# Optimization experiments

Measured on AMD Instinct MI355X. Metric: run time of the kernel, lower is better.

## Reference

```python
import jax, jax.numpy as jnp
import numpy as np
import math

D = 768
H = 8
DK = D // H
FF = 1024
EPS = 1e-5


def _layer_norm(x, g, b):
    m = jnp.mean(x, axis=-1, keepdims=True)
    v = jnp.mean((x - m) ** 2, axis=-1, keepdims=True)
    return (x - m) * jax.lax.rsqrt(v + EPS) * g + b


def _mha(x, attention_mask, Wq, bq, Wv, bv, g, b):
    # x: (B,S,D); attention_mask: (B,S,1) bool (True = masked/padding query row)
    B, S, _ = x.shape
    q = (x @ Wq + bq).reshape(B, S, H, DK).transpose(0, 2, 1, 3)  # (B,H,S,dk)
    # NOTE: original code uses the V projection for BOTH k and v (k = self.V(x))
    kv = (x @ Wv + bv).reshape(B, S, H, DK).transpose(0, 2, 1, 3)
    k = kv
    v = kv
    w = jnp.einsum('bhqd,bhkd->bhqk', q, k) / math.sqrt(DK)  # (B,H,S,S)
    pad = attention_mask[:, None, :, :]                      # (B,1,S,1) -> bcast (B,1,S,S)
    causal = jnp.triu(jnp.ones((S, S), dtype=bool), k=1)     # look-ahead mask
    mask = pad | causal
    w = jnp.where(mask, jnp.float32(-1e9), w)
    # NOTE: original uses nn.Softmax(dim=2) -> softmax over the QUERY axis
    score = jax.nn.softmax(w, axis=2)
    o = jnp.einsum('bhqk,bhkd->bhqd', score, v)              # (B,H,S,dk)
    o = o.transpose(0, 2, 1, 3).reshape(B, S, D)
    return _layer_norm(o + x, g, b)


def _ffn(x, W1, b1, W2, b2, g, b):
    h = jax.nn.relu(x @ W1 + b1)
    return _layer_norm(h @ W2 + b2 + x, g, b)


def setup_inputs() -> dict:
    key = jax.random.key(0)
    ks = jax.random.split(key, 16)
    B, S = 8, 1024
    sc = 0.02
    inp = {
        'x': jax.random.normal(ks[0], (B, S, D), dtype=jnp.float32),
        'attention_mask': jax.random.randint(ks[1], (B, S, 1), 0, 2).astype(bool),
    }
    for i, pre in enumerate(['a1', 'a2']):
        inp[pre + '_Wq'] = jax.random.normal(ks[2 + 4 * i], (D, D), dtype=jnp.float32) * sc
        inp[pre + '_bq'] = jnp.zeros((D,), dtype=jnp.float32)
        inp[pre + '_Wv'] = jax.random.normal(ks[3 + 4 * i], (D, D), dtype=jnp.float32) * sc
        inp[pre + '_bv'] = jnp.zeros((D,), dtype=jnp.float32)
        inp[pre + '_g'] = jnp.ones((D,), dtype=jnp.float32)
        inp[pre + '_b'] = jnp.zeros((D,), dtype=jnp.float32)
    inp['f_W1'] = jax.random.normal(ks[10], (D, FF), dtype=jnp.float32) * sc
    inp['f_b1'] = jnp.zeros((FF,), dtype=jnp.float32)
    inp['f_W2'] = jax.random.normal(ks[11], (FF, D), dtype=jnp.float32) * sc
    inp['f_b2'] = jnp.zeros((D,), dtype=jnp.float32)
    inp['f_g'] = jnp.ones((D,), dtype=jnp.float32)
    inp['f_b'] = jnp.zeros((D,), dtype=jnp.float32)
    return inp


def reference(x, attention_mask,
              a1_Wq, a1_bq, a1_Wv, a1_bv, a1_g, a1_b,
              a2_Wq, a2_bq, a2_Wv, a2_bv, a2_g, a2_b,
              f_W1, f_b1, f_W2, f_b2, f_g, f_b):
    x = _mha(x, attention_mask, a1_Wq, a1_bq, a1_Wv, a1_bv, a1_g, a1_b)
    x = _mha(x, attention_mask, a2_Wq, a2_bq, a2_Wv, a2_bv, a2_g, a2_b)
    x = _ffn(x, f_W1, f_b1, f_W2, f_b2, f_g, f_b)
    return x
```

## Files before the change

### kernel.cpp

```cpp
#include <hip/hip_runtime.h>
#include <cstddef>

#define BB 8
#define SS 1024
#define DD 768
#define HH 8
#define DKK 96
#define FFF 1024
#define MM (BB*SS)
#define QVW 1536
#define SM_SCALE 0.10206207261596577f
#define NTILES 16
#define NPAIR  136

typedef unsigned short ushort_t;
typedef short short8 __attribute__((ext_vector_type(8)));
typedef float f32x4 __attribute__((ext_vector_type(4)));
typedef ushort_t us4 __attribute__((ext_vector_type(4)));

__device__ __forceinline__ ushort_t f2b(float f) {
    union { float f; unsigned u; } x; x.f = f;
    unsigned r = x.u + 0x7fffu + ((x.u >> 16) & 1u);
    return (ushort_t)(r >> 16);
}
__device__ __forceinline__ float b2f(ushort_t u) {
    union { unsigned u; float f; } x; x.u = ((unsigned)u) << 16;
    return x.f;
}
__device__ __forceinline__ void gload16(const ushort_t* g, void* lds_base) {
    __builtin_amdgcn_global_load_lds(
        (const __attribute__((address_space(1))) unsigned int*)g,
        (__attribute__((address_space(3))) unsigned int*)lds_base, 16, 0, 0);
}

__global__ __launch_bounds__(256) void castWT(
    const float* __restrict__ W, ushort_t* __restrict__ Wt, int K, int N)
{
    __shared__ float T[32][33];
    const int tx = threadIdx.x & 31, ty = threadIdx.x >> 5;
    const int n0 = blockIdx.x * 32, k0 = blockIdx.y * 32;
    #pragma unroll
    for (int r = 0; r < 4; ++r)
        T[ty + 8*r][tx] = W[(size_t)(k0 + ty + 8*r) * N + n0 + tx];
    __syncthreads();
    #pragma unroll
    for (int r = 0; r < 4; ++r)
        Wt[(size_t)(n0 + ty + 8*r) * K + k0 + tx] = f2b(T[tx][ty + 8*r]);
}

__global__ __launch_bounds__(256) void castWT4(
    const float* __restrict__ Wa, const float* __restrict__ Wb,
    const float* __restrict__ Wc, const float* __restrict__ Wd,
    ushort_t* __restrict__ Ta, ushort_t* __restrict__ Tb,
    ushort_t* __restrict__ Tc, ushort_t* __restrict__ Td)
{
    __shared__ float T[32][33];
    const float* W; ushort_t* Wt;
    switch (blockIdx.z) {
        case 0:  W = Wa; Wt = Ta; break;
        case 1:  W = Wb; Wt = Tb; break;
        case 2:  W = Wc; Wt = Tc; break;
        default: W = Wd; Wt = Td; break;
    }
    const int tx = threadIdx.x & 31, ty = threadIdx.x >> 5;
    const int n0 = blockIdx.x * 32, k0 = blockIdx.y * 32;
    #pragma unroll
    for (int r = 0; r < 4; ++r)
        T[ty + 8*r][tx] = W[(size_t)(k0 + ty + 8*r) * DD + n0 + tx];
    __syncthreads();
    #pragma unroll
    for (int r = 0; r < 4; ++r)
        Wt[(size_t)(n0 + ty + 8*r) * DD + k0 + tx] = f2b(T[tx][ty + 8*r]);
}

__global__ __launch_bounds__(256) void cast_f2b(
    const float* __restrict__ in, ushort_t* __restrict__ out, int n4)
{
    const int i = blockIdx.x * 256 + threadIdx.x;
    if (i >= n4) return;
    const float4 v = ((const float4*)in)[i];
    us4 o; o.x = f2b(v.x); o.y = f2b(v.y); o.z = f2b(v.z); o.w = f2b(v.w);
    ((us4*)out)[i] = o;
}

template<int RELU>
__global__ __launch_bounds__(256) void gemm_bt(
    const ushort_t* __restrict__ A, const ushort_t* __restrict__ Bt,
    const float* __restrict__ bias, const float* __restrict__ bias2, int bN,
    ushort_t* __restrict__ C, int K, int N)
{
    __shared__ ushort_t S[128*136];
    ushort_t* As = S;
    ushort_t* Bs = S + 128*64;
    const int tid  = threadIdx.x;
    const int lane = tid & 63, wave = tid >> 6;
    const int wm = wave >> 1, wn = wave & 1;
    const int n = lane & 15, quad = lane >> 4;
    const int sx = n & 7;
    const int bm = blockIdx.y * 128, bn = blockIdx.x * 128;

    f32x4 acc[4][4];
    #pragma unroll
    for (int i = 0; i < 4; ++i)
        #pragma unroll
        for (int j = 0; j < 4; ++j) acc[i][j] = (f32x4){0.f, 0.f, 0.f, 0.f};

    for (int k0 = 0; k0 < K; k0 += 64) {
        #pragma unroll
        for (int it = 0; it < 4; ++it) {
            const int u   = (it*4 + wave)*64 + lane;
            const int row = u >> 3;
            const int c   = (u & 7) ^ (row & 7);
            gload16(A  + (size_t)(bm + row) * K + k0 + c*8, (char*)As + (it*4 + wave)*1024);
            gload16(Bt + (size_t)(bn + row) * K + k0 + c*8, (char*)Bs + (it*4 + wave)*1024);
        }
        __syncthreads();
        #pragma unroll
        for (int ks = 0; ks < 2; ++ks) {
            short8 af[4], bf[4];
            #pragma unroll
            for (int i = 0; i < 4; ++i)
                af[i] = *(short8*)&As[((wm*64 + i*16 + n)*8 + ((ks*4 + quad) ^ sx))*8];
            #pragma unroll
            for (int j = 0; j < 4; ++j)
                bf[j] = *(short8*)&Bs[((wn*64 + j*16 + n)*8 + ((ks*4 + quad) ^ sx))*8];
            #pragma unroll
            for (int i = 0; i < 4; ++i)
                #pragma unroll
                for (int j = 0; j < 4; ++j)
                    acc[i][j] = __builtin_amdgcn_mfma_f32_16x16x32_bf16(af[i], bf[j], acc[i][j], 0, 0, 0);
        }
        __syncthreads();
    }
    #pragma unroll
    for (int j = 0; j < 4; ++j) {
        const int col = wn*64 + j*16 + n;
        const int gcol = bn + col;
        const float bsv = (gcol < bN) ? bias[gcol] : bias2[gcol - bN];
        #pragma unroll
        for (int i = 0; i < 4; ++i) {
            const int lrow = wm*64 + i*16 + quad*4;
            #pragma unroll
            for (int r = 0; r < 4; ++r) {
                float v = acc[i][j][r] + bsv;
                if (RELU) v = fmaxf(v, 0.f);
                S[(lrow + r)*136 + col] = f2b(v);
            }
        }
    }
    __syncthreads();
    #pragma unroll
    for (int it = 0; it < 8; ++it) {
        const int u = it*256 + tid;
        const int grow = u >> 4, gc = u & 15;
        *(short8*)(C + (size_t)(bm + grow)*N + bn + gc*8) = *(short8*)&S[grow*136 + gc*8];
    }
}

__global__ __launch_bounds__(256) void attn_sums(
    const ushort_t* __restrict__ QV, const int* __restrict__ amask,
    float* __restrict__ lpart)
{
    __shared__ ushort_t Qs[64*128];
    __shared__ ushort_t Ks[64*128];
    __shared__ float colsum[4][64];
    __shared__ float padf[64];
    const int tid = threadIdx.x, lane = tid & 63, wave = tid >> 6;
    const int n = lane & 15, quad = lane >> 4;
    const int sx = n & 7;
    const int t = blockIdx.x;
    int qt = (int)((-1.f + sqrtf(1.f + 8.f*(float)t)) * 0.5f);
    if ((qt+1)*(qt+2)/2 <= t) ++qt;
    if (qt*(qt+1)/2 > t) --qt;
    const int kt = t - qt*(qt+1)/2;
    const int q0 = qt*64, k0 = kt*64;
    const int h = blockIdx.y, b = blockIdx.z;
    const ushort_t* Qh = QV + (size_t)b*SS*QVW + h*DKK;
    const ushort_t* Kh = QV + (size_t)b*SS*QVW + DD + h*DKK;

    #pragma unroll
    for (int it = 0; it < 4; ++it) {
        const int u = (it*4 + wave)*64 + lane;
        const int row = u >> 4;
        const int c = (u & 15) ^ (row & 7);
        if (c < 12) {
            gload16(Qh + (size_t)(q0 + row)*QVW + c*8, (char*)Qs + (it*4 + wave)*1024);
            gload16(Kh + (size_t)(k0 + row)*QVW + c*8, (char*)Ks + (it*4 + wave)*1024);
        }
    }
    if (tid < 64) padf[tid] = (amask[b*SS + q0 + tid] != 0) ? 1.f : 0.f;
    __syncthreads();

    #pragma unroll
    for (int ns = 0; ns < 4; ++ns) {
        f32x4 sa = (f32x4){0.f, 0.f, 0.f, 0.f};
        #pragma unroll
        for (int ks = 0; ks < 3; ++ks) {
            const short8 aq = *(short8*)&Qs[((wave*16 + n)*16 + ((ks*4 + quad) ^ sx))*8];
            const short8 bk = *(short8*)&Ks[((ns*16   + n)*16 + ((ks*4 + quad) ^ sx))*8];
            sa = __builtin_amdgcn_mfma_f32_16x16x32_bf16(aq, bk, sa, 0, 0, 0);
        }
        const int kl = ns*16 + n;
        const int keyg = k0 + kl;
        float s = 0.f;
        #pragma unroll
        for (int r = 0; r < 4; ++r) {
            const int qrow = wave*16 + quad*4 + r;
            const bool dead = (padf[qrow] != 0.f) || (keyg > q0 + qrow);
            const float e = dead ? 0.f : __expf(sa[r] * SM_SCALE);
            s += e;
        }
        s += __shfl_xor(s, 16);
        s += __shfl_xor(s, 32);
        if (quad == 0) colsum[wave][kl] = s;
    }
    __syncthreads();
    if (tid < 64) {
        const float s = colsum[0][tid] + colsum[1][tid] + colsum[2][tid] + colsum[3][tid];
        lpart[((size_t)(b*HH + h)*NTILES + qt)*SS + k0 + tid] = s;
    }
}

__global__ __launch_bounds__(256) void transpose_scale(
    const ushort_t* __restrict__ QV, const float* __restrict__ lpart,
    ushort_t* __restrict__ Vt)
{
    __shared__ ushort_t T[64][104];
    __shared__ float rlv[64];
    const int tid = threadIdx.x;
    const int k0 = blockIdx.x * 64, h = blockIdx.y, b = blockIdx.z;
    const ushort_t* src = QV + (size_t)b*SS*QVW + DD + h*DKK;
    for (int s = tid; s < 768; s += 256) {
        const int r = s / 12, c = s % 12;
        *(short8*)&T[r][c*8] = *(const short8*)(src + (size_t)(k0 + r)*QVW + c*8);
    }
    if (tid < 64) {
        const float* lp = lpart + (size_t)(b*HH + h)*NTILES*SS;
        float l = 0.f;
        for (int qt = k0 >> 6; qt < NTILES; ++qt) l += lp[(size_t)qt*SS + k0 + tid];
        rlv[tid] = (l > 0.f) ? (1.f / l) : 0.f;
    }
    __syncthreads();
    ushort_t* dst = Vt + ((size_t)b*HH + h)*DKK*SS;
    for (int s = tid; s < 768; s += 256) {
        const int dk = s >> 3, c = s & 7;
        short8 v;
        #pragma unroll
        for (int i = 0; i < 8; ++i)
            v[i] = (short)f2b(b2f(T[c*8 + i][dk]) * rlv[c*8 + i]);
        *(short8*)(dst + (size_t)dk*SS + k0 + c*8) = v;
    }
}

__global__ __launch_bounds__(256) void attn_pv_re(
    const ushort_t* __restrict__ QV, const int* __restrict__ amask,
    const ushort_t* __restrict__ Vt, ushort_t* __restrict__ O)
{
    __shared__ ushort_t Qs[64*128];
    __shared__ ushort_t Ks[64*128];
    __shared__ ushort_t Vs[96*64];
    __shared__ ushort_t Es[64*64];
    __shared__ float padf[64];
    const int tid = threadIdx.x, lane = tid & 63, wave = tid >> 6;
    const int n = lane & 15, quad = lane >> 4;
    const int sx = n & 7;
    const int px = blockIdx.x;
    const int h = blockIdx.y, b = blockIdx.z;
    const ushort_t* Qh = QV + (size_t)b*SS*QVW + h*DKK;
    const ushort_t* Kh = QV + (size_t)b*SS*QVW + DD + h*DKK;
    const ushort_t* Vth = Vt + ((size_t)b*HH + h)*DKK*SS;

    #pragma unroll
    for (int half = 0; half < 2; ++half) {
        const int qt = half ? (15 - px) : px;
        const int q0 = qt * 64;

        #pragma unroll
        for (int it = 0; it < 4; ++it) {
            const int u = (it*4 + wave)*64 + lane;
            const int row = u >> 4;
            const int c = (u & 15) ^ (row & 7);
            if (c < 12)
                gload16(Qh + (size_t)(q0 + row)*QVW + c*8, (char*)Qs + (it*4 + wave)*1024);
        }
        if (tid < 64) padf[tid] = (amask[b*SS + q0 + tid] != 0) ? 1.f : 0.f;

        f32x4 acc[6];
        #pragma unroll
        for (int t = 0; t < 6; ++t) acc[t] = (f32x4){0.f, 0.f, 0.f, 0.f};

        for (int kt = 0; kt <= qt; ++kt) {
            const int k0 = kt * 64;
            #pragma unroll
            for (int it = 0; it < 4; ++it) {
                const int u = (it*4 + wave)*64 + lane;
                const int row = u >> 4;
                const int c = (u & 15) ^ (row & 7);
                if (c < 12)
                    gload16(Kh + (size_t)(k0 + row)*QVW + c*8, (char*)Ks + (it*4 + wave)*1024);
            }
            #pragma unroll
            for (int it = 0; it < 3; ++it) {
                const int u = (it*4 + wave)*64 + lane;
                const int row = u >> 3, c = (u & 7) ^ (row & 7);
                gload16(Vth + (size_t)row*SS + k0 + c*8, (char*)Vs + (it*4 + wave)*1024);
            }
            __syncthreads();

            #pragma unroll
            for (int ns = 0; ns < 4; ++ns) {
                f32x4 sa = (f32x4){0.f, 0.f, 0.f, 0.f};
                #pragma unroll
                for (int ks = 0; ks < 3; ++ks) {
                    const short8 aq = *(short8*)&Qs[((wave*16 + n)*16 + ((ks*4 + quad) ^ sx))*8];
                    const short8 bk = *(short8*)&Ks[((ns*16   + n)*16 + ((ks*4 + quad) ^ sx))*8];
                    sa = __builtin_amdgcn_mfma_f32_16x16x32_bf16(aq, bk, sa, 0, 0, 0);
                }
                const int kl = ns*16 + n;
                const int keyg = k0 + kl;
                #pragma unroll
                for (int r = 0; r < 4; ++r) {
                    const int lq = quad*4 + r;
                    const int trow = wave*16 + lq;
                    const bool dead = (padf[trow] != 0.f) || (keyg > q0 + trow);
                    const float e = dead ? 0.f : __expf(sa[r] * SM_SCALE);
                    Es[trow*64 + (((kl >> 3) ^ (lq & 7)) * 8) + (kl & 7)] = f2b(e);
                }
            }
            asm volatile("s_waitcnt lgkmcnt(0)" ::: "memory");
            __builtin_amdgcn_sched_barrier(0);

            #pragma unroll
            for (int kk = 0; kk < 2; ++kk) {
                const short8 ae = *(short8*)&Es[((wave*16 + n)*8 + ((kk*4 + quad) ^ sx))*8];
                #pragma unroll
                for (int nt = 0; nt < 6; ++nt) {
                    const short8 bv = *(short8*)&Vs[((nt*16 + n)*8 + ((kk*4 + quad) ^ sx))*8];
                    acc[nt] = __builtin_amdgcn_mfma_f32_16x16x32_bf16(ae, bv, acc[nt], 0, 0, 0);
                }
            }
            __syncthreads();
        }
        #pragma unroll
        for (int nt = 0; nt < 6; ++nt) {
            #pragma unroll
            for (int r = 0; r < 4; ++r) {
                const int q = q0 + wave*16 + quad*4 + r;
                O[((size_t)b*SS + q)*DD + h*DKK + nt*16 + n] = f2b(acc[nt][r]);
            }
        }
    }
}

__device__ __forceinline__ float block_sum256(float s, float* tmp4)
{
    #pragma unroll
    for (int off = 32; off > 0; off >>= 1) s += __shfl_down(s, off);
    __syncthreads();
    if ((threadIdx.x & 63) == 0) tmp4[threadIdx.x >> 6] = s;
    __syncthreads();
    return tmp4[0] + tmp4[1] + tmp4[2] + tmp4[3];
}

template<int XBF, int RBF, int OUTF32>
__global__ __launch_bounds__(256) void resid_ln(
    const void* __restrict__ X, const void* __restrict__ R,
    const float* __restrict__ g, const float* __restrict__ beta,
    ushort_t* __restrict__ OutB, float* __restrict__ OutF)
{
    __shared__ float tmp4[4];
    const int row = blockIdx.x;
    const int tid = threadIdx.x;
    float v[3], s = 0.f;
    #pragma unroll
    for (int i = 0; i < 3; ++i) {
        const size_t idx = (size_t)row * DD + tid + 256*i;
        const float xv = XBF ? b2f(((const ushort_t*)X)[idx]) : ((const float*)X)[idx];
        const float rv = RBF ? b2f(((const ushort_t*)R)[idx]) : ((const float*)R)[idx];
        v[i] = xv + rv;
        s += v[i];
    }
    const float mu = block_sum256(s, tmp4) * (1.f / DD);
    float qv = 0.f;
    #pragma unroll
    for (int i = 0; i < 3; ++i) { const float d = v[i] - mu; qv += d * d; }
    const float inv = rsqrtf(block_sum256(qv, tmp4) * (1.f / DD) + 1e-5f);
    #pragma unroll
    for (int i = 0; i < 3; ++i) {
        const int c = tid + 256*i;
        const float o = (v[i] - mu) * inv * g[c] + beta[c];
        if (OUTF32) OutF[(size_t)row * DD + c] = o;
        else        OutB[(size_t)row * DD + c] = f2b(o);
    }
}

extern "C" void kernel_launch(void* const* d_in, const int* in_sizes, int n_in,
                              void* d_out, int out_size, void* d_ws, size_t ws_size,
                              hipStream_t stream)
{
    (void)in_sizes; (void)n_in; (void)out_size; (void)ws_size;
    const float* x0    = (const float*)d_in[0];
    const int*   amask = (const int*)d_in[1];
    const float* a1_Wq = (const float*)d_in[2];
    const float* a1_bq = (const float*)d_in[3];
    const float* a1_Wv = (const float*)d_in[4];
    const float* a1_bv = (const float*)d_in[5];
    const float* a1_g  = (const float*)d_in[6];
    const float* a1_b  = (const float*)d_in[7];
    const float* a2_Wq = (const float*)d_in[8];
    const float* a2_bq = (const float*)d_in[9];
    const float* a2_Wv = (const float*)d_in[10];
    const float* a2_bv = (const float*)d_in[11];
    const float* a2_g  = (const float*)d_in[12];
    const float* a2_b  = (const float*)d_in[13];
    const float* f_W1  = (const float*)d_in[14];
    const float* f_b1  = (const float*)d_in[15];
    const float* f_W2  = (const float*)d_in[16];
    const float* f_b2  = (const float*)d_in[17];
    const float* f_g   = (const float*)d_in[18];
    const float* f_b   = (const float*)d_in[19];

    char* ws = (char*)d_ws;
    size_t off = 0;
    auto alloc = [&](size_t bytes) { void* p = ws + off; off += (bytes + 255) & ~(size_t)255; return p; };
    ushort_t* WqvT1 = (ushort_t*)alloc((size_t)QVW*DD*2);
    ushort_t* WqvT2 = (ushort_t*)alloc((size_t)QVW*DD*2);
    ushort_t* W1T   = (ushort_t*)alloc((size_t)DD*FFF*2);
    ushort_t* W2T   = (ushort_t*)alloc((size_t)DD*FFF*2);
    ushort_t* xb0   = (ushort_t*)alloc((size_t)MM*DD*2);
    ushort_t* xb1   = (ushort_t*)alloc((size_t)MM*DD*2);
    ushort_t* xb2   = (ushort_t*)alloc((size_t)MM*DD*2);
    ushort_t* Ob    = (ushort_t*)alloc((size_t)MM*DD*2);
    ushort_t* QVb   = (ushort_t*)alloc((size_t)MM*QVW*2);
    ushort_t* hb    = QVb;
    ushort_t* Vtb   = (ushort_t*)alloc((size_t)MM*DD*2);
    float* lpart = (float*)alloc((size_t)BB*HH*NTILES*SS*4);
    float* out = (float*)d_out;

    const dim3 blk(256);
    const dim3 gsc(NPAIR, HH, BB);
    const dim3 gpv(NTILES/2, HH, BB);
    const dim3 gtr(SS/64, HH, BB);
    const dim3 gqv(QVW/128, MM/128);
    const dim3 gf1(FFF/128, MM/128);
    const dim3 gf2(DD/128, MM/128);

    castWT4<<<dim3(DD/32, DD/32, 4), blk, 0, stream>>>(
        a1_Wq, a1_Wv, a2_Wq, a2_Wv,
        WqvT1, WqvT1 + (size_t)DD*DD, WqvT2, WqvT2 + (size_t)DD*DD);
    castWT<<<dim3(FFF/32, DD/32), blk, 0, stream>>>(f_W1, W1T, DD, FFF);
    castWT<<<dim3(DD/32, FFF/32), blk, 0, stream>>>(f_W2, W2T, FFF, DD);
    cast_f2b<<<(MM*DD/4 + 255)/256, blk, 0, stream>>>(x0, xb0, MM*DD/4);

    gemm_bt<0><<<gqv, blk, 0, stream>>>(xb0, WqvT1, a1_bq, a1_bv, DD, QVb, DD, QVW);
    attn_sums<<<gsc, blk, 0, stream>>>(QVb, amask, lpart);
    transpose_scale<<<gtr, blk, 0, stream>>>(QVb, lpart, Vtb);
    attn_pv_re<<<gpv, blk, 0, stream>>>(QVb, amask, Vtb, Ob);
    resid_ln<1,0,0><<<dim3(MM), blk, 0, stream>>>(Ob, x0, a1_g, a1_b, xb1, nullptr);

    gemm_bt<0><<<gqv, blk, 0, stream>>>(xb1, WqvT2, a2_bq, a2_bv, DD, QVb, DD, QVW);
    attn_sums<<<gsc, blk, 0, stream>>>(QVb, amask, lpart);
    transpose_scale<<<gtr, blk, 0, stream>>>(QVb, lpart, Vtb);
    attn_pv_re<<<gpv, blk, 0, stream>>>(QVb, amask, Vtb, Ob);
    resid_ln<1,1,0><<<dim3(MM), blk, 0, stream>>>(Ob, xb1, a2_g, a2_b, xb2, nullptr);

    gemm_bt<1><<<gf1, blk, 0, stream>>>(xb2, W1T, f_b1, f_b1, FFF, hb, DD, FFF);
    gemm_bt<0><<<gf2, blk, 0, stream>>>(hb, W2T, f_b2, f_b2, DD, Ob, FFF, DD);
    resid_ln<1,1,1><<<dim3(MM), blk, 0, stream>>>(Ob, xb2, f_g, f_b, nullptr, out);
}
```

Before: 433.1 us.

## Use 128-row query tiles with double-buffered K/V loads in attention kernels

Both attention kernels now process 128-query tiles with 512-thread blocks. Each block loops over 64-key tiles, double-buffering the K and V shared-memory loads so the next tile is fetched while the current one is computed. attn_sums moves from one block per (q,k) tile pair to a looped, paired causal schedule that matches attn_pv_re, with blockIdx remapped to spread heads across XCDs. This halves the partial-sum tiles and reuses Q fragments held in registers, at the cost of more LDS per block and possibly lower occupancy and fewer blocks (256).

```diff
diff --git a/kernel.cpp b/kernel.cpp
--- a/kernel.cpp
+++ b/kernel.cpp
@@ -10,8 +10,7 @@
 #define MM (BB*SS)
 #define QVW 1536
 #define SM_SCALE 0.10206207261596577f
-#define NTILES 16
-#define NPAIR  136
+#define NT2 8
 
 typedef unsigned short ushort_t;
 typedef short short8 __attribute__((ext_vector_type(8)));
@@ -157,67 +156,101 @@
     }
 }
 
-__global__ __launch_bounds__(256) void attn_sums(
+__global__ __launch_bounds__(512) void attn_sums(
     const ushort_t* __restrict__ QV, const int* __restrict__ amask,
     float* __restrict__ lpart)
 {
-    __shared__ ushort_t Qs[64*128];
-    __shared__ ushort_t Ks[64*128];
-    __shared__ float colsum[4][64];
-    __shared__ float padf[64];
+    __shared__ ushort_t Qs[128*128];
+    __shared__ ushort_t Ks[2][64*128];
+    __shared__ float colsum[2][8][64];
     const int tid = threadIdx.x, lane = tid & 63, wave = tid >> 6;
-    const int n = lane & 15, quad = lane >> 4;
-    const int sx = n & 7;
-    const int t = blockIdx.x;
-    int qt = (int)((-1.f + sqrtf(1.f + 8.f*(float)t)) * 0.5f);
-    if ((qt+1)*(qt+2)/2 <= t) ++qt;
-    if (qt*(qt+1)/2 > t) --qt;
-    const int kt = t - qt*(qt+1)/2;
-    const int q0 = qt*64, k0 = kt*64;
-    const int h = blockIdx.y, b = blockIdx.z;
+    const int n = lane & 15, quad = lane >> 4, sx = n & 7;
+    const int hwid = blockIdx.x;
+    const int v = (hwid & 7) * 32 + (hwid >> 3);
+    const int px = v & 3, h = (v >> 2) & 7, b = v >> 5;
     const ushort_t* Qh = QV + (size_t)b*SS*QVW + h*DKK;
     const ushort_t* Kh = QV + (size_t)b*SS*QVW + DD + h*DKK;
-
-    #pragma unroll
-    for (int it = 0; it < 4; ++it) {
-        const int u = (it*4 + wave)*64 + lane;
-        const int row = u >> 4;
-        const int c = (u & 15) ^ (row & 7);
-        if (c < 12) {
-            gload16(Qh + (size_t)(q0 + row)*QVW + c*8, (char*)Qs + (it*4 + wave)*1024);
-            gload16(Kh + (size_t)(k0 + row)*QVW + c*8, (char*)Ks + (it*4 + wave)*1024);
-        }
-    }
-    if (tid < 64) padf[tid] = (amask[b*SS + q0 + tid] != 0) ? 1.f : 0.f;
-    __syncthreads();
-
-    #pragma unroll
-    for (int ns = 0; ns < 4; ++ns) {
-        f32x4 sa = (f32x4){0.f, 0.f, 0.f, 0.f};
-        #pragma unroll
-        for (int ks = 0; ks < 3; ++ks) {
-            const short8 aq = *(short8*)&Qs[((wave*16 + n)*16 + ((ks*4 + quad) ^ sx))*8];
-            const short8 bk = *(short8*)&Ks[((ns*16   + n)*16 + ((ks*4 + quad) ^ sx))*8];
-            sa = __builtin_amdgcn_mfma_f32_16x16x32_bf16(aq, bk, sa, 0, 0, 0);
-        }
-        const int kl = ns*16 + n;
-        const int keyg = k0 + kl;
-        float s = 0.f;
-        #pragma unroll
-        for (int r = 0; r < 4; ++r) {
-            const int qrow = wave*16 + quad*4 + r;
-            const bool dead = (padf[qrow] != 0.f) || (keyg > q0 + qrow);
-            const float e = dead ? 0.f : __expf(sa[r] * SM_SCALE);
-            s += e;
-        }
-        s += __shfl_xor(s, 16);
-        s += __shfl_xor(s, 32);
-        if (quad == 0) colsum[wave][kl] = s;
-    }
-    __syncthreads();
-    if (tid < 64) {
-        const float s = colsum[0][tid] + colsum[1][tid] + colsum[2][tid] + colsum[3][tid];
-        lpart[((size_t)(b*HH + h)*NTILES + qt)*SS + k0 + tid] = s;
+    float* lpq = lpart + (size_t)(b*HH + h)*NT2*SS;
+
+    #pragma unroll
+    for (int half = 0; half < 2; ++half) {
+        const int qt2 = half ? (7 - px) : px;
+        const int q0 = qt2 * 128;
+        const int ktmax = 2*qt2 + 1;
+        #pragma unroll
+        for (int it = 0; it < 4; ++it) {
+            const int u = (it*8 + wave)*64 + lane;
+            const int row = u >> 4, c = (u & 15) ^ (row & 7);
+            if (c < 12)
+                gload16(Qh + (size_t)(q0 + row)*QVW + c*8, (char*)Qs + (it*8 + wave)*1024);
+        }
+        const int4 mv = *(const int4*)&amask[b*SS + q0 + wave*16 + quad*4];
+        const int mr[4] = {mv.x, mv.y, mv.z, mv.w};
+        #pragma unroll
+        for (int it = 0; it < 2; ++it) {
+            const int u = (it*8 + wave)*64 + lane;
+            const int row = u >> 4, c = (u & 15) ^ (row & 7);
+            if (c < 12)
+                gload16(Kh + (size_t)row*QVW + c*8, (char*)Ks[0] + (it*8 + wave)*1024);
+        }
+        __syncthreads();
+        short8 aq[3];
+        #pragma unroll
+        for (int ks = 0; ks < 3; ++ks)
+            aq[ks] = *(short8*)&Qs[((wave*16 + n)*16 + ((ks*4 + quad) ^ sx))*8];
+
+        int cur = 0;
+        for (int kt = 0; kt <= ktmax; ++kt) {
+            const int k0 = kt * 64;
+            if (kt < ktmax) {
+                #pragma unroll
+                for (int it = 0; it < 2; ++it) {
+                    const int u = (it*8 + wave)*64 + lane;
+                    const int row = u >> 4, c = (u & 15) ^ (row & 7);
+                    if (c < 12)
+                        gload16(Kh + (size_t)(k0 + 64 + row)*QVW + c*8,
+                                (char*)Ks[cur^1] + (it*8 + wave)*1024);
+                }
+            }
+            if (kt > 0 && tid < 64) {
+                const float s = colsum[cur^1][0][tid] + colsum[cur^1][1][tid]
+                              + colsum[cur^1][2][tid] + colsum[cur^1][3][tid]
+                              + colsum[cur^1][4][tid] + colsum[cur^1][5][tid]
+                              + colsum[cur^1][6][tid] + colsum[cur^1][7][tid];
+                lpq[(size_t)qt2*SS + (k0 - 64) + tid] = s;
+            }
+            #pragma unroll
+            for (int ns = 0; ns < 4; ++ns) {
+                f32x4 sa = (f32x4){0.f, 0.f, 0.f, 0.f};
+                #pragma unroll
+                for (int ks = 0; ks < 3; ++ks) {
+                    const short8 bk = *(short8*)&Ks[cur][((ns*16 + n)*16 + ((ks*4 + quad) ^ sx))*8];
+                    sa = __builtin_amdgcn_mfma_f32_16x16x32_bf16(aq[ks], bk, sa, 0, 0, 0);
+                }
+                const int kl = ns*16 + n;
+                const int keyg = k0 + kl;
+                float s = 0.f;
+                #pragma unroll
+                for (int r = 0; r < 4; ++r) {
+                    const int qg = q0 + wave*16 + quad*4 + r;
+                    const bool dead = (mr[r] != 0) || (keyg > qg);
+                    s += dead ? 0.f : __expf(sa[r] * SM_SCALE);
+                }
+                s += __shfl_xor(s, 16);
+                s += __shfl_xor(s, 32);
+                if (quad == 0) colsum[cur][wave][kl] = s;
+            }
+            __syncthreads();
+            cur ^= 1;
+        }
+        if (tid < 64) {
+            const int pb = ktmax & 1;
+            const float s = colsum[pb][0][tid] + colsum[pb][1][tid]
+                          + colsum[pb][2][tid] + colsum[pb][3][tid]
+                          + colsum[pb][4][tid] + colsum[pb][5][tid]
+                          + colsum[pb][6][tid] + colsum[pb][7][tid];
+            lpq[(size_t)qt2*SS + ktmax*64 + tid] = s;
+        }
     }
 }
 
@@ -235,9 +268,9 @@
         *(short8*)&T[r][c*8] = *(const short8*)(src + (size_t)(k0 + r)*QVW + c*8);
     }
     if (tid < 64) {
-        const float* lp = lpart + (size_t)(b*HH + h)*NTILES*SS;
+        const float* lp = lpart + (size_t)(b*HH + h)*NT2*SS;
         float l = 0.f;
-        for (int qt = k0 >> 6; qt < NTILES; ++qt) l += lp[(size_t)qt*SS + k0 + tid];
+        for (int qt2 = k0 >> 7; qt2 < NT2; ++qt2) l += lp[(size_t)qt2*SS + k0 + tid];
         rlv[tid] = (l > 0.f) ? (1.f / l) : 0.f;
     }
     __syncthreads();
@@ -252,69 +285,91 @@
     }
 }
 
-__global__ __launch_bounds__(256) void attn_pv_re(
+__global__ __launch_bounds__(512) void attn_pv_re(
     const ushort_t* __restrict__ QV, const int* __restrict__ amask,
     const ushort_t* __restrict__ Vt, ushort_t* __restrict__ O)
 {
-    __shared__ ushort_t Qs[64*128];
-    __shared__ ushort_t Ks[64*128];
-    __shared__ ushort_t Vs[96*64];
-    __shared__ ushort_t Es[64*64];
-    __shared__ float padf[64];
+    __shared__ ushort_t Qs[128*128];
+    __shared__ ushort_t Ks[2][64*128];
+    __shared__ ushort_t Vs[2][96*64];
+    __shared__ ushort_t Es[128*64];
     const int tid = threadIdx.x, lane = tid & 63, wave = tid >> 6;
-    const int n = lane & 15, quad = lane >> 4;
-    const int sx = n & 7;
-    const int px = blockIdx.x;
-    const int h = blockIdx.y, b = blockIdx.z;
+    const int n = lane & 15, quad = lane >> 4, sx = n & 7;
+    const int hwid = blockIdx.x;
+    const int v = (hwid & 7) * 32 + (hwid >> 3);
+    const int px = v & 3, h = (v >> 2) & 7, b = v >> 5;
     const ushort_t* Qh = QV + (size_t)b*SS*QVW + h*DKK;
     const ushort_t* Kh = QV + (size_t)b*SS*QVW + DD + h*DKK;
     const ushort_t* Vth = Vt + ((size_t)b*HH + h)*DKK*SS;
 
     #pragma unroll
     for (int half = 0; half < 2; ++half) {
-        const int qt = half ? (15 - px) : px;
-        const int q0 = qt * 64;
-
+        const int qt2 = half ? (7 - px) : px;
+        const int q0 = qt2 * 128;
+        const int ktmax = 2*qt2 + 1;
         #pragma unroll
         for (int it = 0; it < 4; ++it) {
-            const int u = (it*4 + wave)*64 + lane;
-            const int row = u >> 4;
-            const int c = (u & 15) ^ (row & 7);
+            const int u = (it*8 + wave)*64 + lane;
+            const int row = u >> 4, c = (u & 15) ^ (row & 7);
             if (c < 12)
-                gload16(Qh + (size_t)(q0 + row)*QVW + c*8, (char*)Qs + (it*4 + wave)*1024);
-        }
-        if (tid < 64) padf[tid] = (amask[b*SS + q0 + tid] != 0) ? 1.f : 0.f;
+                gload16(Qh + (size_t)(q0 + row)*QVW + c*8, (char*)Qs + (it*8 + wave)*1024);
+        }
+        const int4 mv = *(const int4*)&amask[b*SS + q0 + wave*16 + quad*4];
+        const int mr[4] = {mv.x, mv.y, mv.z, mv.w};
+        #pragma unroll
+        for (int it = 0; it < 2; ++it) {
+            const int u = (it*8 + wave)*64 + lane;
+            const int row = u >> 4, c = (u & 15) ^ (row & 7);
+            if (c < 12)
+                gload16(Kh + (size_t)row*QVW + c*8, (char*)Ks[0] + (it*8 + wave)*1024);
+        }
+        #pragma unroll
+        for (int it = 0; it < 2; ++it) {
+            if (it*8 + wave < 12) {
+                const int u = (it*8 + wave)*64 + lane;
+                const int row = u >> 3, c = (u & 7) ^ (row & 7);
+                gload16(Vth + (size_t)row*SS + c*8, (char*)Vs[0] + (it*8 + wave)*1024);
+            }
+        }
+        __syncthreads();
+        short8 aq[3];
+        #pragma unroll
+        for (int ks = 0; ks < 3; ++ks)
+            aq[ks] = *(short8*)&Qs[((wave*16 + n)*16 + ((ks*4 + quad) ^ sx))*8];
 
         f32x4 acc[6];
         #pragma unroll
         for (int t = 0; t < 6; ++t) acc[t] = (f32x4){0.f, 0.f, 0.f, 0.f};
 
-        for (int kt = 0; kt <= qt; ++kt) {
+        int cur = 0;
+        for (int kt = 0; kt <= ktmax; ++kt) {
             const int k0 = kt * 64;
-            #pragma unroll
-            for (int it = 0; it < 4; ++it) {
-                const int u = (it*4 + wave)*64 + lane;
-                const int row = u >> 4;
-                const int c = (u & 15) ^ (row & 7);
-                if (c < 12)
-                    gload16(Kh + (size_t)(k0 + row)*QVW + c*8, (char*)Ks + (it*4 + wave)*1024);
-            }
-            #pragma unroll
-            for (int it = 0; it < 3; ++it) {
-                const int u = (it*4 + wave)*64 + lane;
-                const int row = u >> 3, c = (u & 7) ^ (row & 7);
-                gload16(Vth + (size_t)row*SS + k0 + c*8, (char*)Vs + (it*4 + wave)*1024);
-            }
-            __syncthreads();
-
+            if (kt < ktmax) {
+                #pragma unroll
+                for (int it = 0; it < 2; ++it) {
+                    const int u = (it*8 + wave)*64 + lane;
+                    const int row = u >> 4, c = (u & 15) ^ (row & 7);
+                    if (c < 12)
+                        gload16(Kh + (size_t)(k0 + 64 + row)*QVW + c*8,
+                                (char*)Ks[cur^1] + (it*8 + wave)*1024);
+                }
+                #pragma unroll
+                for (int it = 0; it < 2; ++it) {
+                    if (it*8 + wave < 12) {
+                        const int u = (it*8 + wave)*64 + lane;
+                        const int row = u >> 3, c = (u & 7) ^ (row & 7);
+                        gload16(Vth + (size_t)row*SS + k0 + 64 + c*8,
+                                (char*)Vs[cur^1] + (it*8 + wave)*1024);
+                    }
+                }
+            }
             #pragma unroll
             for (int ns = 0; ns < 4; ++ns) {
                 f32x4 sa = (f32x4){0.f, 0.f, 0.f, 0.f};
                 #pragma unroll
                 for (int ks = 0; ks < 3; ++ks) {
-                    const short8 aq = *(short8*)&Qs[((wave*16 + n)*16 + ((ks*4 + quad) ^ sx))*8];
-                    const short8 bk = *(short8*)&Ks[((ns*16   + n)*16 + ((ks*4 + quad) ^ sx))*8];
-                    sa = __builtin_amdgcn_mfma_f32_16x16x32_bf16(aq, bk, sa, 0, 0, 0);
+                    const short8 bk = *(short8*)&Ks[cur][((ns*16 + n)*16 + ((ks*4 + quad) ^ sx))*8];
+                    sa = __builtin_amdgcn_mfma_f32_16x16x32_bf16(aq[ks], bk, sa, 0, 0, 0);
                 }
                 const int kl = ns*16 + n;
                 const int keyg = k0 + kl;
@@ -322,7 +377,7 @@
                 for (int r = 0; r < 4; ++r) {
                     const int lq = quad*4 + r;
                     const int trow = wave*16 + lq;
-                    const bool dead = (padf[trow] != 0.f) || (keyg > q0 + trow);
+                    const bool dead = (mr[r] != 0) || (keyg > q0 + trow);
                     const float e = dead ? 0.f : __expf(sa[r] * SM_SCALE);
                     Es[trow*64 + (((kl >> 3) ^ (lq & 7)) * 8) + (kl & 7)] = f2b(e);
                 }
@@ -335,11 +390,12 @@
                 const short8 ae = *(short8*)&Es[((wave*16 + n)*8 + ((kk*4 + quad) ^ sx))*8];
                 #pragma unroll
                 for (int nt = 0; nt < 6; ++nt) {
-                    const short8 bv = *(short8*)&Vs[((nt*16 + n)*8 + ((kk*4 + quad) ^ sx))*8];
+                    const short8 bv = *(short8*)&Vs[cur][((nt*16 + n)*8 + ((kk*4 + quad) ^ sx))*8];
                     acc[nt] = __builtin_amdgcn_mfma_f32_16x16x32_bf16(ae, bv, acc[nt], 0, 0, 0);
                 }
             }
             __syncthreads();
+            cur ^= 1;
         }
         #pragma unroll
         for (int nt = 0; nt < 6; ++nt) {
@@ -434,12 +490,12 @@
     ushort_t* QVb   = (ushort_t*)alloc((size_t)MM*QVW*2);
     ushort_t* hb    = QVb;
     ushort_t* Vtb   = (ushort_t*)alloc((size_t)MM*DD*2);
-    float* lpart = (float*)alloc((size_t)BB*HH*NTILES*SS*4);
+    float* lpart = (float*)alloc((size_t)BB*HH*NT2*SS*4);
     float* out = (float*)d_out;
 
     const dim3 blk(256);
-    const dim3 gsc(NPAIR, HH, BB);
-    const dim3 gpv(NTILES/2, HH, BB);
+    const dim3 blk512(512);
+    const dim3 gat(256);
     const dim3 gtr(SS/64, HH, BB);
     const dim3 gqv(QVW/128, MM/128);
     const dim3 gf1(FFF/128, MM/128);
@@ -453,15 +509,15 @@
     cast_f2b<<<(MM*DD/4 + 255)/256, blk, 0, stream>>>(x0, xb0, MM*DD/4);
 
     gemm_bt<0><<<gqv, blk, 0, stream>>>(xb0, WqvT1, a1_bq, a1_bv, DD, QVb, DD, QVW);
-    attn_sums<<<gsc, blk, 0, stream>>>(QVb, amask, lpart);
+    attn_sums<<<gat, blk512, 0, stream>>>(QVb, amask, lpart);
     transpose_scale<<<gtr, blk, 0, stream>>>(QVb, lpart, Vtb);
-    attn_pv_re<<<gpv, blk, 0, stream>>>(QVb, amask, Vtb, Ob);
+    attn_pv_re<<<gat, blk512, 0, stream>>>(QVb, amask, Vtb, Ob);
     resid_ln<1,0,0><<<dim3(MM), blk, 0, stream>>>(Ob, x0, a1_g, a1_b, xb1, nullptr);
 
     gemm_bt<0><<<gqv, blk, 0, stream>>>(xb1, WqvT2, a2_bq, a2_bv, DD, QVb, DD, QVW);
-    attn_sums<<<gsc, blk, 0, stream>>>(QVb, amask, lpart);
+    attn_sums<<<gat, blk512, 0, stream>>>(QVb, amask, lpart);
     transpose_scale<<<gtr, blk, 0, stream>>>(QVb, lpart, Vtb);
-    attn_pv_re<<<gpv, blk, 0, stream>>>(QVb, amask, Vtb, Ob);
+    attn_pv_re<<<gat, blk512, 0, stream>>>(QVb, amask, Vtb, Ob);
     resid_ln<1,1,0><<<dim3(MM), blk, 0, stream>>>(Ob, xb1, a2_g, a2_b, xb2, nullptr);
 
     gemm_bt<1><<<gf1, blk, 0, stream>>>(xb2, W1T, f_b1, f_b1, FFF, hb, DD, FFF);
```

After: 387.9 us. -10.4%, faster.
